# Performance work log

Measured on AMD Instinct MI355X. Metric: run time of the kernel, lower is better.

Reference implementation:

```python
import jax, jax.numpy as jnp
import numpy as np

S, IN_DIM = 16384, 1024
NUM_PROJ, PROJ_DIM, BINS = 100, 64, 20
D = NUM_PROJ * PROJ_DIM
EPS = 1e-12  # F.normalize eps


def setup_inputs() -> dict:
    key = jax.random.key(0)
    kx, kw = jax.random.split(key)
    x = jax.random.normal(kx, (S, IN_DIM), dtype=jnp.float32)
    W = jax.random.normal(kw, (D, IN_DIM), dtype=jnp.float32)  # nn.Linear weight, std=1.0 init
    # mins/maxs as produced by cal_min_max over the data (per projected dim)
    proj = x @ W.T
    mins = jnp.min(proj, axis=0)
    maxs = jnp.max(proj, axis=0)
    return {"x": x, "W": W, "mins": mins, "maxs": maxs,
            "num_of_projection": NUM_PROJ, "bins": BINS}


def reference(x, W, mins, maxs, num_of_projection, bins):
    # get_global_feature(x, normalize=True), all histograms fused via scatter-add
    proj = x @ W.T                                   # [S, D]
    d = proj.shape[1]
    proj_dim = d // num_of_projection
    width = maxs - mins                              # [D]
    # torch.histc semantics: values in [min, max] counted; value == max -> last bin
    idx = jnp.floor((proj - mins) / width * bins).astype(jnp.int32)
    idx = jnp.clip(idx, 0, bins - 1)
    valid = (proj >= mins) & (proj <= maxs)
    flat = idx + jnp.arange(d, dtype=jnp.int32)[None, :] * bins   # [S, D]
    hist = jnp.zeros(d * bins, dtype=proj.dtype).at[flat.reshape(-1)].add(
        valid.reshape(-1).astype(proj.dtype))
    gv = hist.reshape(num_of_projection, proj_dim, bins)
    # F.normalize(p=2, dim=2)
    norm = jnp.linalg.norm(gv, axis=2, keepdims=True)
    gv = gv / jnp.maximum(norm, EPS)
    return gv
```

## Files before the change

### kernel.cpp

```cpp
#include <hip/hip_runtime.h>
#include <cmath>

#define S_DIM 16384
#define K_DIM 1024
#define D_DIM 6400
#define NBINS 20
#define HSTRIDE 21

using half_t = _Float16;
using half8  = __attribute__((ext_vector_type(8))) _Float16;
using f32x4  = __attribute__((ext_vector_type(4))) float;

__global__ __launch_bounds__(256) void cvt_fused(
    const float4* __restrict__ x4, unsigned long long* __restrict__ xh8, int n4x,
    const float4* __restrict__ w4, unsigned long long* __restrict__ wh8, int n4w,
    float4* __restrict__ z, int nz4) {
  const int stride = gridDim.x * blockDim.x;
  int tid = blockIdx.x * blockDim.x + threadIdx.x;
  for (int i = tid; i < nz4; i += stride)
    z[i] = (float4){0.f, 0.f, 0.f, 0.f};
  for (int i = tid; i < n4x; i += stride) {
    float4 v = x4[i];
    union { half_t h[4]; unsigned long long u; } c;
    c.h[0] = (half_t)v.x; c.h[1] = (half_t)v.y;
    c.h[2] = (half_t)v.z; c.h[3] = (half_t)v.w;
    xh8[i] = c.u;
  }
  for (int i = tid; i < n4w; i += stride) {
    float4 v = w4[i];
    union { half_t h[4]; unsigned long long u; } c;
    c.h[0] = (half_t)v.x; c.h[1] = (half_t)v.y;
    c.h[2] = (half_t)v.z; c.h[3] = (half_t)v.w;
    wh8[i] = c.u;
  }
}

#define VMWAIT0() __asm__ volatile("s_waitcnt vmcnt(0)" ::: "memory")
#define BAR()     __asm__ volatile("s_barrier" ::: "memory")
#define SP1()     __builtin_amdgcn_s_setprio(1)
#define SP0()     __builtin_amdgcn_s_setprio(0)

#define GLL(SRC, DST) __builtin_amdgcn_global_load_lds(                      \
    (const __attribute__((address_space(1))) void*)(SRC),                    \
    (__attribute__((address_space(3))) void*)(DST), 16, 0, 0)

__global__ __launch_bounds__(1024, 4) void gemm_hist256(
    const half_t* __restrict__ xh, const half_t* __restrict__ wh,
    const float* __restrict__ mins, const float* __restrict__ maxs,
    int* __restrict__ ghist)
{
  __shared__ __align__(16) char ldsA[2 * 32768];
  __shared__ __align__(16) char ldsB[2 * 32768];
  __shared__ int shist[256 * HSTRIDE];

  const int t    = threadIdx.x;
  const int lane = t & 63;
  const int wv   = t >> 6;
  const int wm   = wv >> 2;
  const int wn   = wv & 3;
  const int l16  = lane & 15;
  const int quad = lane >> 4;

  const int bid = blockIdx.x;
  const int wg  = (bid & 7) * 200 + (bid >> 3);
  const int ct  = wg / 64;
  const int rt  = wg - ct * 64;
  const int colBase = ct * 256;
  const int rowBase = rt * 256;

  for (int i = t; i < 256 * HSTRIDE; i += 1024) shist[i] = 0;

  const char* pA0 = ldsA + (wm * 64 + l16) * 128 + (((0 + quad) ^ (l16 & 7)) * 16);
  const char* pA1 = ldsA + (wm * 64 + l16) * 128 + (((4 + quad) ^ (l16 & 7)) * 16);
  const char* pB0 = ldsB + (wn * 64 + l16) * 128 + (((0 + quad) ^ (l16 & 7)) * 16);
  const char* pB1 = ldsB + (wn * 64 + l16) * 128 + (((4 + quad) ^ (l16 & 7)) * 16);

  const int gOff = (t >> 3) * K_DIM + (((t & 7) ^ ((t >> 3) & 7)) * 8);
  const int wvD  = wv * 1024;

  const half_t* xS = xh + (size_t)rowBase * K_DIM + gOff;
  const half_t* wS = wh + (size_t)colBase * K_DIM + gOff;

  f32x4 acc[4][4];
#pragma unroll
  for (int m = 0; m < 4; ++m)
#pragma unroll
    for (int n = 0; n < 4; ++n) acc[m][n] = (f32x4){0.f, 0.f, 0.f, 0.f};

  half8 aF[4], bF[4];

#define MFMA16()                                                             \
  _Pragma("unroll") for (int mf = 0; mf < 4; ++mf)                           \
  _Pragma("unroll") for (int nf = 0; nf < 4; ++nf)                           \
    acc[mf][nf] = __builtin_amdgcn_mfma_f32_16x16x32_f16(                    \
        aF[mf], bF[nf], acc[mf][nf], 0, 0, 0);

  GLL(xS,          ldsA + wvD);
  GLL(xS + 131072, ldsA + 16384 + wvD);
  GLL(wS,          ldsB + wvD);
  GLL(wS + 131072, ldsB + 16384 + wvD);
  VMWAIT0(); BAR();

  const half_t* xStg = xS + 64;
  const half_t* wStg = wS + 64;

#define TILE(PB, PN, STG)                                                    \
  {                                                                          \
    if (STG) {                                                               \
      GLL(xStg,          ldsA + (PN) + wvD);                                 \
      GLL(xStg + 131072, ldsA + (PN) + 16384 + wvD);                         \
      GLL(wStg,          ldsB + (PN) + wvD);                                 \
      GLL(wStg + 131072, ldsB + (PN) + 16384 + wvD);                         \
      xStg += 64; wStg += 64;                                                \
    }                                                                        \
    _Pragma("unroll") for (int mf = 0; mf < 4; ++mf)                         \
      aF[mf] = *(const half8*)(pA0 + (PB) + mf * 2048);                      \
    _Pragma("unroll") for (int nf = 0; nf < 4; ++nf)                         \
      bF[nf] = *(const half8*)(pB0 + (PB) + nf * 2048);                      \
    SP1(); MFMA16(); SP0();                                                  \
    _Pragma("unroll") for (int mf = 0; mf < 4; ++mf)                         \
      aF[mf] = *(const half8*)(pA1 + (PB) + mf * 2048);                      \
    _Pragma("unroll") for (int nf = 0; nf < 4; ++nf)                         \
      bF[nf] = *(const half8*)(pB1 + (PB) + nf * 2048);                      \
    SP1(); MFMA16(); SP0();                                                  \
    VMWAIT0(); BAR();                                                        \
  }

#pragma unroll 1
  for (int it = 0; it < 7; ++it) {
    TILE(0,     32768, 1);
    TILE(32768, 0,     1);
  }
  TILE(0,     32768, 1);
  TILE(32768, 0,     0);

#undef TILE

#pragma unroll
  for (int nf = 0; nf < 4; ++nf) {
    const int lc = wn * 64 + nf * 16 + l16;
    const float a = mins[colBase + lc], b = maxs[colBase + lc];
    const float sc = (float)NBINS / (b - a);
    int* colHist = &shist[lc * HSTRIDE];
#pragma unroll
    for (int mf = 0; mf < 4; ++mf) {
#pragma unroll
      for (int r = 0; r < 4; ++r) {
        float v = acc[mf][nf][r];
        if (v >= a && v <= b) {
          int bin = (int)((v - a) * sc);
          bin = bin > NBINS - 1 ? NBINS - 1 : bin;
          atomicAdd(&colHist[bin], 1);
        }
      }
    }
  }
  __syncthreads();
  for (int i = t; i < 256 * NBINS; i += 1024) {
    int col = i / NBINS, bin = i - col * NBINS;
    int v = shist[col * HSTRIDE + bin];
    if (v) atomicAdd(&ghist[colBase * NBINS + i], v);
  }
}

__global__ __launch_bounds__(256) void gemm_hist_fb(
    const float* __restrict__ xf, const float* __restrict__ wf,
    const float* __restrict__ mins, const float* __restrict__ maxs,
    int* __restrict__ ghist)
{
  __shared__ __align__(16) half_t ldsA[4096];
  __shared__ __align__(16) half_t ldsB[4096];
  __shared__ int shist[128 * HSTRIDE];

  const int t     = threadIdx.x;
  const int lane  = t & 63;
  const int wv    = t >> 6;
  const int waveM = wv >> 1;
  const int waveN = wv & 1;
  const int l16   = lane & 15;
  const int quad  = lane >> 4;
  const int colBase = blockIdx.x * 128;

  for (int i = t; i < 128 * HSTRIDE; i += 256) shist[i] = 0;

  float mn[4], mx[4], inv[4];
  int lcol[4];
#pragma unroll
  for (int nt = 0; nt < 4; ++nt) {
    int lc = waveN * 64 + nt * 16 + l16;
    lcol[nt] = lc;
    float a = mins[colBase + lc], b = maxs[colBase + lc];
    mn[nt] = a; mx[nt] = b;
    inv[nt] = (float)NBINS / (b - a);
  }

  int aOff[4], bOff[4];
#pragma unroll
  for (int mt = 0; mt < 4; ++mt) {
    int m = waveM * 64 + mt * 16 + l16;
    aOff[mt] = (m * 4 + (quad ^ ((m >> 1) & 3))) * 8;
  }
#pragma unroll
  for (int nt = 0; nt < 4; ++nt) {
    int n = waveN * 64 + nt * 16 + l16;
    bOff[nt] = (n * 4 + (quad ^ ((n >> 1) & 3))) * 8;
  }

  for (int rt = blockIdx.y; rt < S_DIM / 128; rt += gridDim.y) {
    const int rowBase = rt * 128;
    f32x4 acc[4][4];
#pragma unroll
    for (int mt = 0; mt < 4; ++mt)
#pragma unroll
      for (int nt = 0; nt < 4; ++nt) acc[mt][nt] = (f32x4){0.f, 0.f, 0.f, 0.f};

    for (int kt = 0; kt < K_DIM; kt += 32) {
      __syncthreads();
#pragma unroll
      for (int i = 0; i < 2; ++i) {
        const int seg = t + i * 256;
        const int row = seg >> 2;
        const int kch = (seg & 3) ^ ((row >> 1) & 3);
        const float* ga = xf + (size_t)(rowBase + row) * K_DIM + kt + kch * 8;
        float4 v0 = ((const float4*)ga)[0];
        float4 v1 = ((const float4*)ga)[1];
        half8 h = { (half_t)v0.x, (half_t)v0.y, (half_t)v0.z, (half_t)v0.w,
                    (half_t)v1.x, (half_t)v1.y, (half_t)v1.z, (half_t)v1.w };
        *(half8*)&ldsA[seg * 8] = h;
        const float* gb = wf + (size_t)(colBase + row) * K_DIM + kt + kch * 8;
        float4 u0 = ((const float4*)gb)[0];
        float4 u1 = ((const float4*)gb)[1];
        half8 g = { (half_t)u0.x, (half_t)u0.y, (half_t)u0.z, (half_t)u0.w,
                    (half_t)u1.x, (half_t)u1.y, (half_t)u1.z, (half_t)u1.w };
        *(half8*)&ldsB[seg * 8] = g;
      }
      __syncthreads();
      {
        half8 aFf[4], bFf[4];
#pragma unroll
        for (int mt = 0; mt < 4; ++mt) aFf[mt] = *(const half8*)&ldsA[aOff[mt]];
#pragma unroll
        for (int nt = 0; nt < 4; ++nt) bFf[nt] = *(const half8*)&ldsB[bOff[nt]];
#pragma unroll
        for (int mt = 0; mt < 4; ++mt)
#pragma unroll
          for (int nt = 0; nt < 4; ++nt)
            acc[mt][nt] = __builtin_amdgcn_mfma_f32_16x16x32_f16(
                aFf[mt], bFf[nt], acc[mt][nt], 0, 0, 0);
      }
    }

#pragma unroll
    for (int nt = 0; nt < 4; ++nt) {
      const float a = mn[nt], b = mx[nt], sc = inv[nt];
      int* colHist = &shist[lcol[nt] * HSTRIDE];
#pragma unroll
      for (int mt = 0; mt < 4; ++mt) {
#pragma unroll
        for (int r = 0; r < 4; ++r) {
          float v = acc[mt][nt][r];
          if (v >= a && v <= b) {
            int bin = (int)((v - a) * sc);
            bin = bin > NBINS - 1 ? NBINS - 1 : bin;
            atomicAdd(&colHist[bin], 1);
          }
        }
      }
    }
  }

  __syncthreads();
  for (int i = t; i < 128 * NBINS; i += 256) {
    int col = i / NBINS, bin = i - col * NBINS;
    int v = shist[col * HSTRIDE + bin];
    if (v) atomicAdd(&ghist[colBase * NBINS + i], v);
  }
}

__global__ void normalize_kernel(const int* __restrict__ hist, float* __restrict__ out) {
  int g = blockIdx.x * blockDim.x + threadIdx.x;
  if (g >= D_DIM) return;
  const int base = g * NBINS;
  float v[NBINS];
  float ss = 0.f;
#pragma unroll
  for (int i = 0; i < NBINS; ++i) { v[i] = (float)hist[base + i]; ss += v[i] * v[i]; }
  float sc = 1.0f / fmaxf(sqrtf(ss), 1e-12f);
#pragma unroll
  for (int i = 0; i < NBINS; ++i) out[base + i] = v[i] * sc;
}

extern "C" void kernel_launch(void* const* d_in, const int* in_sizes, int n_in,
                              void* d_out, int out_size, void* d_ws, size_t ws_size,
                              hipStream_t stream) {
  const float* x    = (const float*)d_in[0];
  const float* W    = (const float*)d_in[1];
  const float* mins = (const float*)d_in[2];
  const float* maxs = (const float*)d_in[3];
  float* out = (float*)d_out;

  const size_t xh_elems = (size_t)S_DIM * K_DIM;
  const size_t wh_elems = (size_t)D_DIM * K_DIM;
  const size_t need = (xh_elems + wh_elems) * sizeof(half_t);

  if (ws_size >= need) {
    half_t* xh = (half_t*)d_ws;
    half_t* wh = xh + xh_elems;
    int n4x = (int)(xh_elems / 4), n4w = (int)(wh_elems / 4);
    cvt_fused<<<2048, 256, 0, stream>>>(
        (const float4*)x, (unsigned long long*)xh, n4x,
        (const float4*)W, (unsigned long long*)wh, n4w,
        (float4*)d_out, out_size / 4);
    gemm_hist256<<<dim3(1600), 1024, 0, stream>>>(xh, wh, mins, maxs, (int*)d_out);
  } else {
    hipMemsetAsync(d_out, 0, (size_t)out_size * sizeof(float), stream);
    gemm_hist_fb<<<dim3(D_DIM / 128, 64), 256, 0, stream>>>(
        x, W, mins, maxs, (int*)d_out);
  }

  normalize_kernel<<<(D_DIM + 255) / 256, 256, 0, stream>>>((int*)d_out, out);
}
```

Baseline: 360.3 us.

## Halve GEMM workgroup to 512 threads and stream B fragments straight to registers

Cuts the fused GEMM+histogram block from 16 waves to 8, so each wave now computes a 128x64 output tile (8x4 MFMA fragments) instead of 64x64. The W operand no longer goes through LDS: each wave loads its B fragments directly from global memory into registers one k-step ahead, while only the A tile is staged through LDS with global_load_lds. The waitcnt is relaxed to vmcnt(8), so the register-bound B loads can stay in flight across the barrier. This roughly halves LDS use and LDS read traffic per block. In exchange, B is read from global/L2 redundantly by the two wave rows, each lane makes scattered 16-byte row loads, and register pressure rises sharply with 128 accumulators plus 16 fragment registers.

```diff
diff --git a/kernel.cpp b/kernel.cpp
--- a/kernel.cpp
+++ b/kernel.cpp
@@ -35,7 +35,7 @@
   }
 }
 
-#define VMWAIT0() __asm__ volatile("s_waitcnt vmcnt(0)" ::: "memory")
+#define VMWAIT(N) __asm__ volatile("s_waitcnt vmcnt(" #N ")" ::: "memory")
 #define BAR()     __asm__ volatile("s_barrier" ::: "memory")
 #define SP1()     __builtin_amdgcn_s_setprio(1)
 #define SP0()     __builtin_amdgcn_s_setprio(0)
@@ -44,13 +44,12 @@
     (const __attribute__((address_space(1))) void*)(SRC),                    \
     (__attribute__((address_space(3))) void*)(DST), 16, 0, 0)
 
-__global__ __launch_bounds__(1024, 4) void gemm_hist256(
+__global__ __launch_bounds__(512, 2) void gemm_hist256(
     const half_t* __restrict__ xh, const half_t* __restrict__ wh,
     const float* __restrict__ mins, const float* __restrict__ maxs,
     int* __restrict__ ghist)
 {
   __shared__ __align__(16) char ldsA[2 * 32768];
-  __shared__ __align__(16) char ldsB[2 * 32768];
   __shared__ int shist[256 * HSTRIDE];
 
   const int t    = threadIdx.x;
@@ -68,71 +67,75 @@
   const int colBase = ct * 256;
   const int rowBase = rt * 256;
 
-  for (int i = t; i < 256 * HSTRIDE; i += 1024) shist[i] = 0;
-
-  const char* pA0 = ldsA + (wm * 64 + l16) * 128 + (((0 + quad) ^ (l16 & 7)) * 16);
-  const char* pA1 = ldsA + (wm * 64 + l16) * 128 + (((4 + quad) ^ (l16 & 7)) * 16);
-  const char* pB0 = ldsB + (wn * 64 + l16) * 128 + (((0 + quad) ^ (l16 & 7)) * 16);
-  const char* pB1 = ldsB + (wn * 64 + l16) * 128 + (((4 + quad) ^ (l16 & 7)) * 16);
+  for (int i = t; i < 256 * HSTRIDE; i += 512) shist[i] = 0;
+
+  const char* pA0 = ldsA + (wm * 128 + l16) * 128 + (((0 + quad) ^ (l16 & 7)) * 16);
+  const char* pA1 = ldsA + (wm * 128 + l16) * 128 + (((4 + quad) ^ (l16 & 7)) * 16);
 
   const int gOff = (t >> 3) * K_DIM + (((t & 7) ^ ((t >> 3) & 7)) * 8);
   const int wvD  = wv * 1024;
-
   const half_t* xS = xh + (size_t)rowBase * K_DIM + gOff;
-  const half_t* wS = wh + (size_t)colBase * K_DIM + gOff;
-
-  f32x4 acc[4][4];
-#pragma unroll
-  for (int m = 0; m < 4; ++m)
+
+  const half_t* wB0 = wh + (size_t)(colBase + wn * 64 +  0 + l16) * K_DIM + quad * 8;
+  const half_t* wB1 = wh + (size_t)(colBase + wn * 64 + 16 + l16) * K_DIM + quad * 8;
+  const half_t* wB2 = wh + (size_t)(colBase + wn * 64 + 32 + l16) * K_DIM + quad * 8;
+  const half_t* wB3 = wh + (size_t)(colBase + wn * 64 + 48 + l16) * K_DIM + quad * 8;
+
+  f32x4 acc[8][4];
+#pragma unroll
+  for (int m = 0; m < 8; ++m)
 #pragma unroll
     for (int n = 0; n < 4; ++n) acc[m][n] = (f32x4){0.f, 0.f, 0.f, 0.f};
 
-  half8 aF[4], bF[4];
-
-#define MFMA16()                                                             \
-  _Pragma("unroll") for (int mf = 0; mf < 4; ++mf)                           \
+  half8 aF[8], bF[8];
+
+#define LOADB()                                                              \
+  {                                                                          \
+    bF[0] = *(const half8*)(wB0);      bF[1] = *(const half8*)(wB1);         \
+    bF[2] = *(const half8*)(wB2);      bF[3] = *(const half8*)(wB3);         \
+    bF[4] = *(const half8*)(wB0 + 32); bF[5] = *(const half8*)(wB1 + 32);    \
+    bF[6] = *(const half8*)(wB2 + 32); bF[7] = *(const half8*)(wB3 + 32);    \
+    wB0 += 64; wB1 += 64; wB2 += 64; wB3 += 64;                              \
+  }
+#define MFMA32(KS)                                                           \
+  _Pragma("unroll") for (int mf = 0; mf < 8; ++mf)                           \
   _Pragma("unroll") for (int nf = 0; nf < 4; ++nf)                           \
     acc[mf][nf] = __builtin_amdgcn_mfma_f32_16x16x32_f16(                    \
-        aF[mf], bF[nf], acc[mf][nf], 0, 0, 0);
-
-  GLL(xS,          ldsA + wvD);
-  GLL(xS + 131072, ldsA + 16384 + wvD);
-  GLL(wS,          ldsB + wvD);
-  GLL(wS + 131072, ldsB + 16384 + wvD);
-  VMWAIT0(); BAR();
-
-  const half_t* xStg = xS + 64;
-  const half_t* wStg = wS + 64;
-
-#define TILE(PB, PN, STG)                                                    \
+        aF[mf], bF[(KS) * 4 + nf], acc[mf][nf], 0, 0, 0);
+#define STAGEA(PN)                                                           \
   {                                                                          \
-    if (STG) {                                                               \
-      GLL(xStg,          ldsA + (PN) + wvD);                                 \
-      GLL(xStg + 131072, ldsA + (PN) + 16384 + wvD);                         \
-      GLL(wStg,          ldsB + (PN) + wvD);                                 \
-      GLL(wStg + 131072, ldsB + (PN) + 16384 + wvD);                         \
-      xStg += 64; wStg += 64;                                                \
-    }                                                                        \
-    _Pragma("unroll") for (int mf = 0; mf < 4; ++mf)                         \
+    GLL(xStg,               ldsA + (PN) +         wvD);                      \
+    GLL(xStg +  64 * K_DIM, ldsA + (PN) +  8192 + wvD);                      \
+    GLL(xStg + 128 * K_DIM, ldsA + (PN) + 16384 + wvD);                      \
+    GLL(xStg + 192 * K_DIM, ldsA + (PN) + 24576 + wvD);                      \
+    xStg += 64;                                                              \
+  }
+
+  const half_t* xStg = xS;
+  STAGEA(0);
+  LOADB();
+  VMWAIT(8); BAR();
+
+#define TILE(PB, PN, STG, DOB, WAITE)                                        \
+  {                                                                          \
+    if (STG) STAGEA(PN);                                                     \
+    _Pragma("unroll") for (int mf = 0; mf < 8; ++mf)                         \
       aF[mf] = *(const half8*)(pA0 + (PB) + mf * 2048);                      \
-    _Pragma("unroll") for (int nf = 0; nf < 4; ++nf)                         \
-      bF[nf] = *(const half8*)(pB0 + (PB) + nf * 2048);                      \
-    SP1(); MFMA16(); SP0();                                                  \
-    _Pragma("unroll") for (int mf = 0; mf < 4; ++mf)                         \
+    SP1(); MFMA32(0); SP0();                                                 \
+    _Pragma("unroll") for (int mf = 0; mf < 8; ++mf)                         \
       aF[mf] = *(const half8*)(pA1 + (PB) + mf * 2048);                      \
-    _Pragma("unroll") for (int nf = 0; nf < 4; ++nf)                         \
-      bF[nf] = *(const half8*)(pB1 + (PB) + nf * 2048);                      \
-    SP1(); MFMA16(); SP0();                                                  \
-    VMWAIT0(); BAR();                                                        \
+    SP1(); MFMA32(1); SP0();                                                 \
+    if (DOB) LOADB();                                                        \
+    WAITE; BAR();                                                            \
   }
 
 #pragma unroll 1
   for (int it = 0; it < 7; ++it) {
-    TILE(0,     32768, 1);
-    TILE(32768, 0,     1);
-  }
-  TILE(0,     32768, 1);
-  TILE(32768, 0,     0);
+    TILE(0,     32768, 1, 1, VMWAIT(8));
+    TILE(32768, 0,     1, 1, VMWAIT(8));
+  }
+  TILE(0,     32768, 1, 1, VMWAIT(8));
+  TILE(32768, 0,     0, 0, VMWAIT(0));
 
 #undef TILE
 
@@ -143,7 +146,7 @@
     const float sc = (float)NBINS / (b - a);
     int* colHist = &shist[lc * HSTRIDE];
 #pragma unroll
-    for (int mf = 0; mf < 4; ++mf) {
+    for (int mf = 0; mf < 8; ++mf) {
 #pragma unroll
       for (int r = 0; r < 4; ++r) {
         float v = acc[mf][nf][r];
@@ -156,7 +159,7 @@
     }
   }
   __syncthreads();
-  for (int i = t; i < 256 * NBINS; i += 1024) {
+  for (int i = t; i < 256 * NBINS; i += 512) {
     int col = i / NBINS, bin = i - col * NBINS;
     int v = shist[col * HSTRIDE + bin];
     if (v) atomicAdd(&ghist[colBase * NBINS + i], v);
@@ -311,7 +314,7 @@
         (const float4*)x, (unsigned long long*)xh, n4x,
         (const float4*)W, (unsigned long long*)wh, n4w,
         (float4*)d_out, out_size / 4);
-    gemm_hist256<<<dim3(1600), 1024, 0, stream>>>(xh, wh, mins, maxs, (int*)d_out);
+    gemm_hist256<<<dim3(1600), 512, 0, stream>>>(xh, wh, mins, maxs, (int*)d_out);
   } else {
     hipMemsetAsync(d_out, 0, (size_t)out_size * sizeof(float), stream);
     gemm_hist_fb<<<dim3(D_DIM / 128, 64), 256, 0, stream>>>(
```

New measurement: 482.2 us. +33.8%, slower.
